# Kernel optimization log

Hardware: AMD Instinct MI355X
Metric: run time of the kernel (lower is better)

The kernel has to match this reference:

```python
import jax, jax.numpy as jnp
import numpy as np

N_NODES = 50000
N_EDGES = 800000
IN_DIM = 256
HID = 128
OUT = 128
LEAKY_SLOPE = 0.01


def setup_inputs() -> dict:
    key = jax.random.key(0)
    ks = jax.random.split(key, 12)
    s = 0.05
    return {
        "h": jax.random.normal(ks[0], (N_NODES, IN_DIM), dtype=jnp.float32),
        "src": jax.random.randint(ks[1], (N_EDGES,), 0, N_NODES, dtype=jnp.int32),
        "dst": jax.random.randint(ks[2], (N_EDGES,), 0, N_NODES, dtype=jnp.int32),
        "W1": jax.random.normal(ks[3], (HID, IN_DIM), dtype=jnp.float32) * s,
        "b1": jax.random.normal(ks[4], (HID,), dtype=jnp.float32) * s,
        "a1": jax.random.normal(ks[5], (2 * HID,), dtype=jnp.float32) * s,
        "ab1": jax.random.normal(ks[6], (), dtype=jnp.float32) * s,
        "W2": jax.random.normal(ks[7], (OUT, HID), dtype=jnp.float32) * s,
        "b2": jax.random.normal(ks[8], (OUT,), dtype=jnp.float32) * s,
        "a2": jax.random.normal(ks[9], (2 * OUT,), dtype=jnp.float32) * s,
        "ab2": jax.random.normal(ks[10], (), dtype=jnp.float32) * s,
    }


def gat_layer(h, src, dst, W, b, a, ab, n_nodes):
    # z = fc(h)
    z = h @ W.T + b                      # [N, D]
    D = z.shape[-1]
    zs = z[src]                           # [E, D] gather src features
    zd = z[dst]                           # [E, D] gather dst features
    # attn_fc(cat[zs, zd]) == zs @ a[:D] + zd @ a[D:] + ab
    e = zs @ a[:D] + zd @ a[D:] + ab      # [E]
    e = jnp.where(e > 0, e, LEAKY_SLOPE * e)  # leaky_relu, slope 0.01
    # segment softmax over edges grouped by destination node
    m = jax.ops.segment_max(e, dst, num_segments=n_nodes)   # [N]
    ex = jnp.exp(e - m[dst])                                  # [E]
    denom = jax.ops.segment_sum(ex, dst, num_segments=n_nodes)  # [N]
    alpha = ex / denom[dst]                                   # [E]
    # weighted scatter-sum of src features into dst nodes
    return jax.ops.segment_sum(alpha[:, None] * zs, dst, num_segments=n_nodes)


def reference(h, src, dst, W1, b1, a1, ab1, W2, b2, a2, ab2):
    n = h.shape[0]
    h1 = jax.nn.elu(gat_layer(h, src, dst, W1, b1, a1, ab1, n))
    h2 = jax.nn.elu(gat_layer(h1, src, dst, W2, b2, a2, ab2, n))
    return h2
```

## Files before the change

kernel.cpp:

```cpp
#include <hip/hip_runtime.h>
#include <hip/hip_bf16.h>

#define N_NODES 50000
#define N_EDGES 800000
#define IN_DIM  256
#define HID     128
#define LEAKY   0.01f

#define EDGE_BLOCKS  ((N_EDGES + 255) / 256)
#define NODE_WBLKS   (N_NODES / 4)
#define SCAN_BLOCKS  ((N_NODES + 255) / 256)
#define W1_ELEMS  (HID * IN_DIM)
#define W2_ELEMS  (HID * HID)

#define TM        64
#define FC_BLOCKS ((N_NODES + TM - 1) / TM)

typedef __attribute__((ext_vector_type(8))) short short8;
typedef __attribute__((ext_vector_type(4))) float f32x4;

__device__ __forceinline__ unsigned short f2bf(float x) {
    union { __hip_bfloat16 b; unsigned short u; } c;
    c.b = __float2bfloat16(x);
    return c.u;
}
__device__ __forceinline__ float bf2f(unsigned short u) {
    union { unsigned int u; float f; } c;
    c.u = ((unsigned int)u) << 16;
    return c.f;
}
__device__ __forceinline__ float2 bfu2(unsigned int u) {
    float2 r;
    r.x = bf2f((unsigned short)(u & 0xffff));
    r.y = bf2f((unsigned short)(u >> 16));
    return r;
}
__device__ __forceinline__ float lky(float x) { return x > 0.f ? x : LEAKY * x; }
__device__ __forceinline__ float rl_f(float v, int l) {
    return __int_as_float(__builtin_amdgcn_readlane(__float_as_int(v), l));
}

__device__ __forceinline__ void cvt8(const float4 v0, const float4 v1,
                                     short8& hi, short8& lo) {
    float f[8] = {v0.x, v0.y, v0.z, v0.w, v1.x, v1.y, v1.z, v1.w};
#pragma unroll
    for (int j = 0; j < 8; j++) {
        unsigned short h = f2bf(f[j]);
        hi[j] = (short)h;
        lo[j] = (short)f2bf(f[j] - bf2f(h));
    }
}


__global__ void hist_split(const int* __restrict__ dst, int* __restrict__ counts,
                           int* __restrict__ erank,
                           const float* __restrict__ W1, unsigned short* __restrict__ w1hi,
                           unsigned short* __restrict__ w1lo,
                           const float* __restrict__ W2, unsigned short* __restrict__ w2hi,
                           unsigned short* __restrict__ w2lo) {
    int i = blockIdx.x * 256 + threadIdx.x;
    if (i < N_EDGES) erank[i] = atomicAdd(&counts[dst[i]], 1);
    if (i < W1_ELEMS) {
        float x = W1[i];
        unsigned short h = f2bf(x);
        w1hi[i] = h;
        w1lo[i] = f2bf(x - bf2f(h));
    } else if (i < W1_ELEMS + W2_ELEMS) {
        int j = i - W1_ELEMS;
        float x = W2[j];
        unsigned short h = f2bf(x);
        w2hi[j] = h;
        w2lo[j] = f2bf(x - bf2f(h));
    }
}

__global__ void scan_block(const int* __restrict__ counts, int* __restrict__ offsets,
                           int* __restrict__ bsums) {
    __shared__ int sh[256];
    int tid = threadIdx.x;
    int i = blockIdx.x * 256 + tid;
    int v = (i < N_NODES) ? counts[i] : 0;
    sh[tid] = v;
    __syncthreads();
    for (int o = 1; o < 256; o <<= 1) {
        int t = (tid >= o) ? sh[tid - o] : 0;
        __syncthreads();
        sh[tid] += t;
        __syncthreads();
    }
    if (i < N_NODES) offsets[i] = sh[tid] - v;
    if (tid == 255) bsums[blockIdx.x] = sh[255];
}

__global__ void scan_add(int* __restrict__ offsets, const int* __restrict__ bsums) {
    __shared__ int sh[256];
    int tid = threadIdx.x;
    int b = blockIdx.x;
    sh[tid] = (tid < b) ? bsums[tid] : 0;
    __syncthreads();
    for (int o = 128; o > 0; o >>= 1) {
        if (tid < o) sh[tid] += sh[tid + o];
        __syncthreads();
    }
    int base = sh[0];
    int i = b * 256 + tid;
    if (i < N_NODES) offsets[i] += base;
    if (i == N_NODES) offsets[N_NODES] = N_EDGES;
}

__global__ void fill_kernel(const int* __restrict__ dst, const int* __restrict__ src,
                            const int* __restrict__ erank,
                            const int* __restrict__ offsets,
                            int* __restrict__ csr_src) {
    int i = blockIdx.x * 256 + threadIdx.x;
    if (i < N_EDGES) {
        int d = dst[i];
        int slot = offsets[d] + erank[i];
        __builtin_nontemporal_store(src[i], &csr_src[slot]);
    }
}


__device__ __forceinline__ void epi(const f32x4* accn, int lrow0, int m0, int q, int lane,
                                    const float* __restrict__ bias,
                                    const float* __restrict__ attn,
                                    unsigned short* __restrict__ Zb,
                                    float* __restrict__ sbuf) {
    int r = lane & 15;
    int lrowbase = lrow0 + (lane >> 4) * 4;
    float ps[4] = {0.f, 0.f, 0.f, 0.f};
    float pd[4] = {0.f, 0.f, 0.f, 0.f};
#pragma unroll
    for (int nt = 0; nt < 4; nt++) {
        int n = q * 64 + nt * 16 + r;
        float bn = bias[n];
        float aS = attn[n];
        float aD = attn[HID + n];
#pragma unroll
        for (int reg = 0; reg < 4; reg++) {
            float zv = accn[nt][reg] + bn;
            if (m0 + lrowbase + reg < N_NODES)
                Zb[(size_t)(m0 + lrowbase + reg) * HID + n] = f2bf(zv);
            ps[reg] += zv * aS;
            pd[reg] += zv * aD;
        }
    }
#pragma unroll
    for (int o = 1; o < 16; o <<= 1) {
#pragma unroll
        for (int reg = 0; reg < 4; reg++) {
            ps[reg] += __shfl_xor(ps[reg], o, 64);
            pd[reg] += __shfl_xor(pd[reg], o, 64);
        }
    }
    if (r == 0) {
#pragma unroll
        for (int reg = 0; reg < 4; reg++) {
            sbuf[q * 128 + lrowbase + reg] = ps[reg];
            sbuf[q * 128 + 64 + lrowbase + reg] = pd[reg];
        }
    }
}

__device__ __forceinline__ void score_combine(const float* __restrict__ sbuf, int tid, int m0,
                                              float* __restrict__ sS, float* __restrict__ sD) {
    if (tid < TM) {
        int gr = m0 + tid;
        if (gr < N_NODES) {
            sS[gr] = sbuf[tid] + sbuf[128 + tid];
            sD[gr] = sbuf[64 + tid] + sbuf[128 + 64 + tid];
        }
    }
}


__launch_bounds__(256, 3)
__global__ void gemm_fc1(const float* __restrict__ A,
                         const unsigned short* __restrict__ Whi,
                         const unsigned short* __restrict__ Wlo,
                         const float* __restrict__ bias,
                         const float* __restrict__ attn,
                         unsigned short* __restrict__ Zb,
                         float* __restrict__ sS, float* __restrict__ sD) {
    __shared__ float sbuf[256];

    int tid  = threadIdx.x;
    int lane = tid & 63;
    int w    = tid >> 6;
    int q    = w & 1;
    int mh   = w >> 1;
    int m0   = blockIdx.x * TM;
    int r    = lane & 15;
    int koff = (lane >> 4) * 8;

    const float* Ap[2];
#pragma unroll
    for (int s = 0; s < 2; s++) {
        int gr = m0 + mh * 32 + s * 16 + r;
        if (gr >= N_NODES) gr = N_NODES - 1;
        Ap[s] = A + (size_t)gr * IN_DIM + koff;
    }
    const unsigned short* Bph = Whi + (size_t)(q * 64 + r) * IN_DIM + koff;
    const unsigned short* Bpl = Wlo + (size_t)(q * 64 + r) * IN_DIM + koff;

    f32x4 acc[2][4];
#pragma unroll
    for (int s = 0; s < 2; s++)
#pragma unroll
        for (int nt = 0; nt < 4; nt++) acc[s][nt] = (f32x4){0.f, 0.f, 0.f, 0.f};

#pragma unroll 2
    for (int kt = 0; kt < IN_DIM / 32; kt++) {
        int k0 = kt * 32;
        short8 ah[2], al[2], bh[4], bl[4];
#pragma unroll
        for (int nt = 0; nt < 4; nt++) {
            bh[nt] = *(const short8*)(Bph + (size_t)nt * 16 * IN_DIM + k0);
            bl[nt] = *(const short8*)(Bpl + (size_t)nt * 16 * IN_DIM + k0);
        }
#pragma unroll
        for (int s = 0; s < 2; s++) {
            float4 v0 = *(const float4*)(Ap[s] + k0);
            float4 v1 = *(const float4*)(Ap[s] + k0 + 4);
            cvt8(v0, v1, ah[s], al[s]);
        }
#pragma unroll
        for (int s = 0; s < 2; s++)
#pragma unroll
            for (int nt = 0; nt < 4; nt++) {
                acc[s][nt] = __builtin_amdgcn_mfma_f32_16x16x32_bf16(ah[s], bh[nt], acc[s][nt], 0, 0, 0);
                acc[s][nt] = __builtin_amdgcn_mfma_f32_16x16x32_bf16(al[s], bh[nt], acc[s][nt], 0, 0, 0);
                acc[s][nt] = __builtin_amdgcn_mfma_f32_16x16x32_bf16(ah[s], bl[nt], acc[s][nt], 0, 0, 0);
            }
    }

#pragma unroll
    for (int s = 0; s < 2; s++)
        epi(acc[s], mh * 32 + s * 16, m0, q, lane, bias, attn, Zb, sbuf);
    __syncthreads();
    score_combine(sbuf, tid, m0, sS, sD);
}


__launch_bounds__(256, 3)
__global__ void gemm_fc2(const unsigned short* __restrict__ Abf,
                         const unsigned short* __restrict__ Whi,
                         const unsigned short* __restrict__ Wlo,
                         const float* __restrict__ bias,
                         const float* __restrict__ attn,
                         unsigned short* __restrict__ Zb,
                         float* __restrict__ sS, float* __restrict__ sD) {
    __shared__ float sbuf[256];

    int tid  = threadIdx.x;
    int lane = tid & 63;
    int w    = tid >> 6;
    int q    = w & 1;
    int mh   = w >> 1;
    int m0   = blockIdx.x * TM;
    int r    = lane & 15;
    int koff = (lane >> 4) * 8;

    const unsigned short* Ap[2];
#pragma unroll
    for (int s = 0; s < 2; s++) {
        int gr = m0 + mh * 32 + s * 16 + r;
        if (gr >= N_NODES) gr = N_NODES - 1;
        Ap[s] = Abf + (size_t)gr * HID + koff;
    }
    const unsigned short* Bph = Whi + (size_t)(q * 64 + r) * HID + koff;
    const unsigned short* Bpl = Wlo + (size_t)(q * 64 + r) * HID + koff;

    f32x4 acc[2][4];
#pragma unroll
    for (int s = 0; s < 2; s++)
#pragma unroll
        for (int nt = 0; nt < 4; nt++) acc[s][nt] = (f32x4){0.f, 0.f, 0.f, 0.f};

#pragma unroll 2
    for (int kt = 0; kt < HID / 32; kt++) {
        int k0 = kt * 32;
        short8 ah[2], bh[4], bl[4];
#pragma unroll
        for (int nt = 0; nt < 4; nt++) {
            bh[nt] = *(const short8*)(Bph + (size_t)nt * 16 * HID + k0);
            bl[nt] = *(const short8*)(Bpl + (size_t)nt * 16 * HID + k0);
        }
#pragma unroll
        for (int s = 0; s < 2; s++)
            ah[s] = *(const short8*)(Ap[s] + k0);
#pragma unroll
        for (int s = 0; s < 2; s++)
#pragma unroll
            for (int nt = 0; nt < 4; nt++) {
                acc[s][nt] = __builtin_amdgcn_mfma_f32_16x16x32_bf16(ah[s], bh[nt], acc[s][nt], 0, 0, 0);
                acc[s][nt] = __builtin_amdgcn_mfma_f32_16x16x32_bf16(ah[s], bl[nt], acc[s][nt], 0, 0, 0);
            }
    }

#pragma unroll
    for (int s = 0; s < 2; s++)
        epi(acc[s], mh * 32 + s * 16, m0, q, lane, bias, attn, Zb, sbuf);
    __syncthreads();
    score_combine(sbuf, tid, m0, sS, sD);
}


template <int OUT_BF>
__launch_bounds__(256)
__global__ void aggregate(const unsigned short* __restrict__ Zb,
                          const int* __restrict__ csr_src,
                          const int* __restrict__ offsets,
                          const float* __restrict__ sS,
                          const float* __restrict__ sD,
                          const float* __restrict__ ab,
                          unsigned short* __restrict__ OutBf,
                          float* __restrict__ OutF) {
    int v = blockIdx.x * 4 + (threadIdx.x >> 6);
    int lane = threadIdx.x & 63;
    int off = offsets[v];
    int deg = offsets[v + 1] - off;
    float sdv = sD[v] + ab[0];

    const unsigned int* Zrow = (const unsigned int*)Zb;
    float2 acc = {0.f, 0.f};

    if (deg <= 64) {
        bool act = lane < deg;
        int s_l = 0;
        float x = -3.0e38f;
        if (act) {
            s_l = csr_src[off + lane];
            x = lky(sS[s_l] + sdv);
        }
        float mx = x;
#pragma unroll
        for (int o = 32; o > 0; o >>= 1) mx = fmaxf(mx, __shfl_xor(mx, o, 64));
        float ex = act ? __expf(x - mx) : 0.f;
        float sum = ex;
#pragma unroll
        for (int o = 32; o > 0; o >>= 1) sum += __shfl_xor(sum, o, 64);
        float al_l = (deg > 0) ? ex / sum : 0.f;

        int t = 0;
        for (; t + 16 <= deg; t += 16) {
            int   s[16];
            float a[16];
            unsigned int rw[16];
#pragma unroll
            for (int j = 0; j < 16; j++) {
                s[j] = __builtin_amdgcn_readlane(s_l, t + j);
                a[j] = rl_f(al_l, t + j);
            }
#pragma unroll
            for (int j = 0; j < 16; j++)
                rw[j] = Zrow[(size_t)s[j] * (HID / 2) + lane];
#pragma unroll
            for (int j = 0; j < 16; j++) {
                float2 zz = bfu2(rw[j]);
                acc.x += a[j] * zz.x;
                acc.y += a[j] * zz.y;
            }
        }
        for (; t + 4 <= deg; t += 4) {
            int   s[4];
            float a[4];
            unsigned int rw[4];
#pragma unroll
            for (int j = 0; j < 4; j++) {
                s[j] = __builtin_amdgcn_readlane(s_l, t + j);
                a[j] = rl_f(al_l, t + j);
            }
#pragma unroll
            for (int j = 0; j < 4; j++)
                rw[j] = Zrow[(size_t)s[j] * (HID / 2) + lane];
#pragma unroll
            for (int j = 0; j < 4; j++) {
                float2 zz = bfu2(rw[j]);
                acc.x += a[j] * zz.x;
                acc.y += a[j] * zz.y;
            }
        }
        for (; t < deg; t++) {
            int sj = __builtin_amdgcn_readlane(s_l, t);
            float aj = rl_f(al_l, t);
            float2 zz = bfu2(Zrow[(size_t)sj * (HID / 2) + lane]);
            acc.x += aj * zz.x;
            acc.y += aj * zz.y;
        }
    } else {
        float mx = -3.0e38f;
        for (int t = lane; t < deg; t += 64) {
            int s = csr_src[off + t];
            mx = fmaxf(mx, lky(sS[s] + sdv));
        }
#pragma unroll
        for (int o = 32; o > 0; o >>= 1) mx = fmaxf(mx, __shfl_xor(mx, o, 64));
        float sum = 0.f;
        for (int t = lane; t < deg; t += 64) {
            int s = csr_src[off + t];
            sum += __expf(lky(sS[s] + sdv) - mx);
        }
#pragma unroll
        for (int o = 32; o > 0; o >>= 1) sum += __shfl_xor(sum, o, 64);
        float inv = 1.f / sum;
        for (int t = 0; t < deg; t++) {
            int s = csr_src[off + t];
            float al = __expf(lky(sS[s] + sdv) - mx) * inv;
            float2 zz = bfu2(Zrow[(size_t)s * (HID / 2) + lane]);
            acc.x += al * zz.x;
            acc.y += al * zz.y;
        }
    }

    acc.x = acc.x > 0.f ? acc.x : __expf(acc.x) - 1.f;
    acc.y = acc.y > 0.f ? acc.y : __expf(acc.y) - 1.f;

    if (OUT_BF) {
        ushort2 o2;
        o2.x = f2bf(acc.x);
        o2.y = f2bf(acc.y);
        *((ushort2*)(OutBf + (size_t)v * HID + lane * 2)) = o2;
    } else {
        float2 o2 = {acc.x, acc.y};
        *((float2*)(OutF + (size_t)v * HID + lane * 2)) = o2;
    }
}


extern "C" void kernel_launch(void* const* d_in, const int* in_sizes, int n_in,
                              void* d_out, int out_size, void* d_ws, size_t ws_size,
                              hipStream_t stream) {
    const float* h   = (const float*)d_in[0];
    const int*   src = (const int*)d_in[1];
    const int*   dst = (const int*)d_in[2];
    const float* W1  = (const float*)d_in[3];
    const float* b1  = (const float*)d_in[4];
    const float* a1  = (const float*)d_in[5];
    const float* ab1 = (const float*)d_in[6];
    const float* W2  = (const float*)d_in[7];
    const float* b2  = (const float*)d_in[8];
    const float* a2  = (const float*)d_in[9];
    const float* ab2 = (const float*)d_in[10];
    float* out = (float*)d_out;

    unsigned short* zb = (unsigned short*)d_ws;
    float* sS = (float*)(zb + (size_t)N_NODES * HID);
    float* sD = sS + N_NODES;
    int* counts  = (int*)(sD + N_NODES);
    int* offsets = counts + N_NODES;
    int* bsums   = offsets + N_NODES + 16;
    unsigned short* h1   = (unsigned short*)(bsums + 256);
    unsigned short* w1hi = h1 + (size_t)N_NODES * HID;
    unsigned short* w1lo = w1hi + W1_ELEMS;
    unsigned short* w2hi = w1lo + W1_ELEMS;
    unsigned short* w2lo = w2hi + W2_ELEMS;
    int* csr_src = (int*)(w2lo + W2_ELEMS);
    int* erank   = csr_src + N_EDGES;

    hipMemsetAsync(counts, 0, (size_t)N_NODES * sizeof(int), stream);

    hist_split<<<EDGE_BLOCKS, 256, 0, stream>>>(dst, counts, erank,
                                                W1, w1hi, w1lo, W2, w2hi, w2lo);
    scan_block<<<SCAN_BLOCKS, 256, 0, stream>>>(counts, offsets, bsums);
    scan_add<<<SCAN_BLOCKS, 256, 0, stream>>>(offsets, bsums);
    fill_kernel<<<EDGE_BLOCKS, 256, 0, stream>>>(dst, src, erank, offsets, csr_src);

    gemm_fc1<<<FC_BLOCKS, 256, 0, stream>>>(h, w1hi, w1lo, b1, a1, zb, sS, sD);
    aggregate<1><<<NODE_WBLKS, 256, 0, stream>>>(zb, csr_src, offsets, sS, sD, ab1, h1, nullptr);

    gemm_fc2<<<FC_BLOCKS, 256, 0, stream>>>(h1, w2hi, w2lo, b2, a2, zb, sS, sD);
    aggregate<0><<<NODE_WBLKS, 256, 0, stream>>>(zb, csr_src, offsets, sS, sD, ab2, nullptr, out);
}
```

Baseline: 313.3 us.

## Double-buffer GEMM operands in LDS via async global_load_lds in both FC kernels

Both FC GEMM kernels now stage A and the split-bf16 weight tiles into a double-buffered shared-memory region with direct global-to-LDS loads. The next k-slice is prefetched while MFMAs run on the current one, and each tile is fetched once per block instead of once per wave. This is meant to hide global-load latency and cut redundant weight traffic. In exchange it uses much more LDS per block (about 48KB and 40KB), drops the occupancy hint from launch bounds, and adds a barrier per k-step.

```diff
diff --git a/kernel.cpp b/kernel.cpp
--- a/kernel.cpp
+++ b/kernel.cpp
@@ -18,6 +18,11 @@
 
 typedef __attribute__((ext_vector_type(8))) short short8;
 typedef __attribute__((ext_vector_type(4))) float f32x4;
+
+#define GLDS(g, l)                                                              \
+    __builtin_amdgcn_global_load_lds(                                           \
+        (const __attribute__((address_space(1))) void*)(g),                     \
+        (__attribute__((address_space(3))) void*)(l), 16, 0, 0)
 
 __device__ __forceinline__ unsigned short f2bf(float x) {
     union { __hip_bfloat16 b; unsigned short u; } c;
@@ -174,7 +179,7 @@
 }
 
 
-__launch_bounds__(256, 3)
+__launch_bounds__(256)
 __global__ void gemm_fc1(const float* __restrict__ A,
                          const unsigned short* __restrict__ Whi,
                          const unsigned short* __restrict__ Wlo,
@@ -182,7 +187,7 @@
                          const float* __restrict__ attn,
                          unsigned short* __restrict__ Zb,
                          float* __restrict__ sS, float* __restrict__ sD) {
-    __shared__ float sbuf[256];
+    __shared__ char lds[2][24576];
 
     int tid  = threadIdx.x;
     int lane = tid & 63;
@@ -191,17 +196,39 @@
     int mh   = w >> 1;
     int m0   = blockIdx.x * TM;
     int r    = lane & 15;
-    int koff = (lane >> 4) * 8;
-
-    const float* Ap[2];
-#pragma unroll
-    for (int s = 0; s < 2; s++) {
-        int gr = m0 + mh * 32 + s * 16 + r;
-        if (gr >= N_NODES) gr = N_NODES - 1;
-        Ap[s] = A + (size_t)gr * IN_DIM + koff;
-    }
-    const unsigned short* Bph = Whi + (size_t)(q * 64 + r) * IN_DIM + koff;
-    const unsigned short* Bpl = Wlo + (size_t)(q * 64 + r) * IN_DIM + koff;
+    int kg   = lane >> 4;
+
+    const char* gp[6];
+    int gstep[6];
+    int loff[6];
+#pragma unroll
+    for (int j = 0; j < 6; j++) {
+        int c = w * 6 + j;
+        loff[j] = c * 1024;
+        if (c < 8) {
+            int S = c >> 1, hh = c & 1;
+            int row = m0 + S * 16 + r;
+            if (row >= N_NODES) row = N_NODES - 1;
+            gp[j] = (const char*)(A + (size_t)row * IN_DIM + kg * 8 + hh * 4);
+            gstep[j] = 32 * 4;
+        } else if (c < 16) {
+            int nt = c - 8;
+            gp[j] = (const char*)(Whi + (size_t)(nt * 16 + r) * IN_DIM + kg * 8);
+            gstep[j] = 32 * 2;
+        } else {
+            int nt = c - 16;
+            gp[j] = (const char*)(Wlo + (size_t)(nt * 16 + r) * IN_DIM + kg * 8);
+            gstep[j] = 32 * 2;
+        }
+    }
+
+#define STAGE1(b)                                                   \
+    {                                                               \
+        _Pragma("unroll") for (int j = 0; j < 6; j++) {             \
+            GLDS(gp[j], lds[b] + loff[j]);                          \
+            gp[j] += gstep[j];                                      \
+        }                                                           \
+    }
 
     f32x4 acc[2][4];
 #pragma unroll
@@ -209,20 +236,30 @@
 #pragma unroll
         for (int nt = 0; nt < 4; nt++) acc[s][nt] = (f32x4){0.f, 0.f, 0.f, 0.f};
 
-#pragma unroll 2
+    STAGE1(0);
+    __syncthreads();
+
+#pragma unroll
     for (int kt = 0; kt < IN_DIM / 32; kt++) {
-        int k0 = kt * 32;
+        const int cur = kt & 1;
+        if (kt < IN_DIM / 32 - 1) STAGE1(cur ^ 1);
+
+        const float* Af = (const float*)lds[cur];
+        const unsigned short* Bh = (const unsigned short*)(lds[cur] + 8192);
+        const unsigned short* Bl = (const unsigned short*)(lds[cur] + 16384);
+
         short8 ah[2], al[2], bh[4], bl[4];
 #pragma unroll
+        for (int s = 0; s < 2; s++) {
+            int S = mh * 2 + s;
+            float4 v0 = *(const float4*)(Af + (S * 2 + 0) * 256 + lane * 4);
+            float4 v1 = *(const float4*)(Af + (S * 2 + 1) * 256 + lane * 4);
+            cvt8(v0, v1, ah[s], al[s]);
+        }
+#pragma unroll
         for (int nt = 0; nt < 4; nt++) {
-            bh[nt] = *(const short8*)(Bph + (size_t)nt * 16 * IN_DIM + k0);
-            bl[nt] = *(const short8*)(Bpl + (size_t)nt * 16 * IN_DIM + k0);
-        }
-#pragma unroll
-        for (int s = 0; s < 2; s++) {
-            float4 v0 = *(const float4*)(Ap[s] + k0);
-            float4 v1 = *(const float4*)(Ap[s] + k0 + 4);
-            cvt8(v0, v1, ah[s], al[s]);
+            bh[nt] = *(const short8*)(Bh + (q * 4 + nt) * 512 + lane * 8);
+            bl[nt] = *(const short8*)(Bl + (q * 4 + nt) * 512 + lane * 8);
         }
 #pragma unroll
         for (int s = 0; s < 2; s++)
@@ -232,8 +269,11 @@
                 acc[s][nt] = __builtin_amdgcn_mfma_f32_16x16x32_bf16(al[s], bh[nt], acc[s][nt], 0, 0, 0);
                 acc[s][nt] = __builtin_amdgcn_mfma_f32_16x16x32_bf16(ah[s], bl[nt], acc[s][nt], 0, 0, 0);
             }
-    }
-
+        __syncthreads();
+    }
+#undef STAGE1
+
+    float* sbuf = (float*)lds[0];
 #pragma unroll
     for (int s = 0; s < 2; s++)
         epi(acc[s], mh * 32 + s * 16, m0, q, lane, bias, attn, Zb, sbuf);
@@ -242,7 +282,7 @@
 }
 
 
-__launch_bounds__(256, 3)
+__launch_bounds__(256)
 __global__ void gemm_fc2(const unsigned short* __restrict__ Abf,
                          const unsigned short* __restrict__ Whi,
                          const unsigned short* __restrict__ Wlo,
@@ -250,7 +290,7 @@
                          const float* __restrict__ attn,
                          unsigned short* __restrict__ Zb,
                          float* __restrict__ sS, float* __restrict__ sD) {
-    __shared__ float sbuf[256];
+    __shared__ char lds[2][20480];
 
     int tid  = threadIdx.x;
     int lane = tid & 63;
@@ -259,17 +299,32 @@
     int mh   = w >> 1;
     int m0   = blockIdx.x * TM;
     int r    = lane & 15;
-    int koff = (lane >> 4) * 8;
-
-    const unsigned short* Ap[2];
-#pragma unroll
-    for (int s = 0; s < 2; s++) {
-        int gr = m0 + mh * 32 + s * 16 + r;
-        if (gr >= N_NODES) gr = N_NODES - 1;
-        Ap[s] = Abf + (size_t)gr * HID + koff;
-    }
-    const unsigned short* Bph = Whi + (size_t)(q * 64 + r) * HID + koff;
-    const unsigned short* Bpl = Wlo + (size_t)(q * 64 + r) * HID + koff;
+    int kg   = lane >> 4;
+
+    const char* gp[5];
+    int loff[5];
+#pragma unroll
+    for (int j = 0; j < 5; j++) {
+        int c = w * 5 + j;
+        loff[j] = c * 1024;
+        if (c < 4) {
+            int row = m0 + c * 16 + r;
+            if (row >= N_NODES) row = N_NODES - 1;
+            gp[j] = (const char*)(Abf + (size_t)row * HID + kg * 8);
+        } else if (c < 12) {
+            gp[j] = (const char*)(Whi + (size_t)((c - 4) * 16 + r) * HID + kg * 8);
+        } else {
+            gp[j] = (const char*)(Wlo + (size_t)((c - 12) * 16 + r) * HID + kg * 8);
+        }
+    }
+
+#define STAGE2(b)                                                   \
+    {                                                               \
+        _Pragma("unroll") for (int j = 0; j < 5; j++) {             \
+            GLDS(gp[j], lds[b] + loff[j]);                          \
+            gp[j] += 64;                                            \
+        }                                                           \
+    }
 
     f32x4 acc[2][4];
 #pragma unroll
@@ -277,27 +332,39 @@
 #pragma unroll
         for (int nt = 0; nt < 4; nt++) acc[s][nt] = (f32x4){0.f, 0.f, 0.f, 0.f};
 
-#pragma unroll 2
+    STAGE2(0);
+    __syncthreads();
+
+#pragma unroll
     for (int kt = 0; kt < HID / 32; kt++) {
-        int k0 = kt * 32;
-        short8 ah[2], bh[4], bl[4];
+        const int cur = kt & 1;
+        if (kt < HID / 32 - 1) STAGE2(cur ^ 1);
+
+        const unsigned short* Aq = (const unsigned short*)lds[cur];
+        const unsigned short* Bh = (const unsigned short*)(lds[cur] + 4096);
+        const unsigned short* Bl = (const unsigned short*)(lds[cur] + 12288);
+
+        short8 a8[2], bh[4], bl[4];
+#pragma unroll
+        for (int s = 0; s < 2; s++)
+            a8[s] = *(const short8*)(Aq + (mh * 2 + s) * 512 + lane * 8);
 #pragma unroll
         for (int nt = 0; nt < 4; nt++) {
-            bh[nt] = *(const short8*)(Bph + (size_t)nt * 16 * HID + k0);
-            bl[nt] = *(const short8*)(Bpl + (size_t)nt * 16 * HID + k0);
+            bh[nt] = *(const short8*)(Bh + (q * 4 + nt) * 512 + lane * 8);
+            bl[nt] = *(const short8*)(Bl + (q * 4 + nt) * 512 + lane * 8);
         }
 #pragma unroll
         for (int s = 0; s < 2; s++)
-            ah[s] = *(const short8*)(Ap[s] + k0);
-#pragma unroll
-        for (int s = 0; s < 2; s++)
 #pragma unroll
             for (int nt = 0; nt < 4; nt++) {
-                acc[s][nt] = __builtin_amdgcn_mfma_f32_16x16x32_bf16(ah[s], bh[nt], acc[s][nt], 0, 0, 0);
-                acc[s][nt] = __builtin_amdgcn_mfma_f32_16x16x32_bf16(ah[s], bl[nt], acc[s][nt], 0, 0, 0);
+                acc[s][nt] = __builtin_amdgcn_mfma_f32_16x16x32_bf16(a8[s], bh[nt], acc[s][nt], 0, 0, 0);
+                acc[s][nt] = __builtin_amdgcn_mfma_f32_16x16x32_bf16(a8[s], bl[nt], acc[s][nt], 0, 0, 0);
             }
-    }
-
+        __syncthreads();
+    }
+#undef STAGE2
+
+    float* sbuf = (float*)lds[0];
 #pragma unroll
     for (int s = 0; s < 2; s++)
         epi(acc[s], mh * 32 + s * 16, m0, q, lane, bias, attn, Zb, sbuf);
```

New measurement: 287.6 us. 8.2% less time.
